# Optimization experiments

Measured on AMD Instinct MI355X. Metric: run time of the kernel, lower is better.

Reference implementation:

```python
import jax, jax.numpy as jnp
import numpy as np


def setup_inputs() -> dict:
    key = jax.random.key(0)
    k_x, k_adj, k_w1, k_b1, k_w2, k_b2 = jax.random.split(key, 6)
    B, S, N, HD = 16, 2048, 64, 32
    x = jax.random.normal(k_x, (B, S, N), dtype=jnp.float32)
    adj = jax.random.uniform(k_adj, (N, N), dtype=jnp.float32)
    # module forces diagonal to 1.0 at init
    adj = adj.at[jnp.arange(N), jnp.arange(N)].set(1.0)
    fc1_w = jax.random.normal(k_w1, (HD, 1), dtype=jnp.float32) * (1.0 / np.sqrt(1.0))
    fc1_b = jax.random.normal(k_b1, (HD,), dtype=jnp.float32) * 0.02
    fc2_w = jax.random.normal(k_w2, (HD, 2 * HD), dtype=jnp.float32) * (1.0 / np.sqrt(2 * HD))
    fc2_b = jax.random.normal(k_b2, (HD,), dtype=jnp.float32) * 0.02
    return {"x": x, "adj": adj, "fc1_w": fc1_w, "fc1_b": fc1_b,
            "fc2_w": fc2_w, "fc2_b": fc2_b}


def reference(x, adj, fc1_w, fc1_b, fc2_w, fc2_b):
    B, S, N = x.shape
    HD = fc1_w.shape[0]
    # row-normalized adjacency
    adj_norm = adj / (adj.sum(axis=1, keepdims=True) + 1e-8)  # [N, N]
    # fc1: Linear(1 -> HD) on x[..., None]; equivalent to outer product + bias
    h = jax.nn.relu(x[..., None] * fc1_w[:, 0] + fc1_b)       # [B, S, N, HD]
    # adjacency-weighted aggregation over variables
    agg = jnp.einsum('ij,bsjf->bsif', adj_norm, h)            # [B, S, N, HD]
    # fc2: Linear(2*HD -> HD) on concat([h, agg])
    h2 = jax.nn.relu(jnp.concatenate([h, agg], axis=-1) @ fc2_w.T + fc2_b)  # [B, S, N, HD]
    # AdaptiveAvgPool1d(1) over seq after permute(0,2,3,1).reshape(B, N*HD, S)
    z = h2.mean(axis=1).reshape(B, N * HD)                    # [B, N*HD]
    return z
```

## Files before the change

kernel.cpp:

```cpp
#include <hip/hip_runtime.h>

#define BN 16
#define SN 2048
#define NV 64
#define HD 32
#define TCH 8
#define SCHUNK 64
#define NSUB (SCHUNK / TCH)
#define CATP 40

typedef short  bf8_t  __attribute__((ext_vector_type(8)));
typedef __bf16 bfv8   __attribute__((ext_vector_type(8)));
typedef __bf16 bfv4   __attribute__((ext_vector_type(4)));
typedef float  f32x16 __attribute__((ext_vector_type(16)));

#define MFMA32(a, b, c) __builtin_amdgcn_mfma_f32_32x32x16_bf16( \
    __builtin_bit_cast(bf8_t, (a)), __builtin_bit_cast(bf8_t, (b)), (c), 0, 0, 0)

__global__ __launch_bounds__(256, 2) void gnn_mfma(
    const float* __restrict__ x,
    const float* __restrict__ adj,
    const float* __restrict__ w1,
    const float* __restrict__ b1,
    const float* __restrict__ w2,
    const float* __restrict__ b2,
    float* __restrict__ out)
{
    __shared__ float  xs[TCH][NV];
    __shared__ __bf16 catg[TCH][NV][CATP];
    __shared__ float  red[NV * HD];
    __shared__ float  rs[NV];

    const int tid  = threadIdx.x;
    const int w    = tid >> 6;
    const int lane = tid & 63;
    const int l31  = lane & 31;
    const int lh   = lane >> 5;
    const int b    = blockIdx.x >> 5;
    const int chk  = blockIdx.x & 31;
    const int sbase = chk * SCHUNK;

    #pragma unroll
    for (int q = 0; q < (NV * HD) / 256; ++q) red[tid + q * 256] = 0.f;

    if (tid < NV) {
        float s = 0.f;
        const float4* r4 = (const float4*)(adj + tid * NV);
        #pragma unroll
        for (int q = 0; q < NV / 4; ++q) { float4 v = r4[q]; s += v.x + v.y + v.z + v.w; }
        rs[tid] = 1.f / (s + 1e-8f);
    }
    __syncthreads();

    bfv8 an[2][4];
    #pragma unroll
    for (int nt = 0; nt < 2; ++nt) {
        const int i = nt * 32 + l31;
        const float rsi = rs[i];
        #pragma unroll
        for (int kk = 0; kk < 4; ++kk) {
            const int j0 = kk * 16 + lh * 8;
            const float4 a0 = *(const float4*)(adj + i * NV + j0);
            const float4 a1 = *(const float4*)(adj + i * NV + j0 + 4);
            bfv8 v;
            v[0] = (__bf16)(a0.x * rsi); v[1] = (__bf16)(a0.y * rsi);
            v[2] = (__bf16)(a0.z * rsi); v[3] = (__bf16)(a0.w * rsi);
            v[4] = (__bf16)(a1.x * rsi); v[5] = (__bf16)(a1.y * rsi);
            v[6] = (__bf16)(a1.z * rsi); v[7] = (__bf16)(a1.w * rsi);
            an[nt][kk] = v;
        }
    }

    bfv8 wf[4];
    #pragma unroll
    for (int kk = 0; kk < 4; ++kk) {
        const int k0 = kk * 16 + lh * 8;
        const float4 a0 = *(const float4*)(w2 + l31 * (2 * HD) + k0);
        const float4 a1 = *(const float4*)(w2 + l31 * (2 * HD) + k0 + 4);
        bfv8 v;
        v[0] = (__bf16)a0.x; v[1] = (__bf16)a0.y; v[2] = (__bf16)a0.z; v[3] = (__bf16)a0.w;
        v[4] = (__bf16)a1.x; v[5] = (__bf16)a1.y; v[6] = (__bf16)a1.z; v[7] = (__bf16)a1.w;
        wf[kk] = v;
    }

    const float w1f = w1[l31];
    const float b1f = b1[l31];
    const float b2f = b2[l31];
    float w1k[2][8], b1k[2][8];
    #pragma unroll
    for (int kk = 0; kk < 2; ++kk) {
        const int k0 = kk * 16 + lh * 8;
        #pragma unroll
        for (int e = 0; e < 8; ++e) { w1k[kk][e] = w1[k0 + e]; b1k[kk][e] = b1[k0 + e]; }
    }

    f32x16 macc0, macc1;
    #pragma unroll
    for (int r = 0; r < 16; ++r) { macc0[r] = 0.f; macc1[r] = 0.f; }

    for (int t = 0; t < NSUB; ++t) {
        __syncthreads();
        if (tid < 128) {
            ((float4*)&xs[0][0])[tid] =
                ((const float4*)(x + ((size_t)b * SN + sbase + t * TCH) * (size_t)NV))[tid];
        }
        __syncthreads();

        #pragma unroll
        for (int sp = 0; sp < 2; ++sp) {
            const int sl = 2 * w + sp;
            bfv8 a1f[4];
            #pragma unroll
            for (int kk = 0; kk < 4; ++kk) {
                const int j0 = kk * 16 + lh * 8;
                const float4 xa = *(const float4*)&xs[sl][j0];
                const float4 xb = *(const float4*)&xs[sl][j0 + 4];
                bfv8 v;
                v[0] = (__bf16)fmaxf(xa.x * w1f + b1f, 0.f);
                v[1] = (__bf16)fmaxf(xa.y * w1f + b1f, 0.f);
                v[2] = (__bf16)fmaxf(xa.z * w1f + b1f, 0.f);
                v[3] = (__bf16)fmaxf(xa.w * w1f + b1f, 0.f);
                v[4] = (__bf16)fmaxf(xb.x * w1f + b1f, 0.f);
                v[5] = (__bf16)fmaxf(xb.y * w1f + b1f, 0.f);
                v[6] = (__bf16)fmaxf(xb.z * w1f + b1f, 0.f);
                v[7] = (__bf16)fmaxf(xb.w * w1f + b1f, 0.f);
                a1f[kk] = v;
            }
            #pragma unroll
            for (int nt = 0; nt < 2; ++nt) {
                f32x16 c;
                #pragma unroll
                for (int r = 0; r < 16; ++r) c[r] = 0.f;
                #pragma unroll
                for (int kk = 0; kk < 4; ++kk) c = MFMA32(a1f[kk], an[nt][kk], c);
                const int i = nt * 32 + l31;
                #pragma unroll
                for (int g = 0; g < 4; ++g) {
                    const int f0 = g * 8 + 4 * lh;
                    bfv4 pv;
                    pv[0] = (__bf16)c[g * 4 + 0]; pv[1] = (__bf16)c[g * 4 + 1];
                    pv[2] = (__bf16)c[g * 4 + 2]; pv[3] = (__bf16)c[g * 4 + 3];
                    *(bfv4*)&catg[sl][i][f0] = pv;
                }
            }
        }

        #pragma unroll
        for (int p = 0; p < 4; ++p) {
            const int mt = 4 * w + p;
            const int sl = mt >> 1;
            const int ih = mt & 1;
            const int i  = ih * 32 + l31;
            const float xv = xs[sl][i];
            f32x16 c;
            #pragma unroll
            for (int r = 0; r < 16; ++r) c[r] = 0.f;
            #pragma unroll
            for (int kk = 0; kk < 2; ++kk) {
                bfv8 v;
                #pragma unroll
                for (int e = 0; e < 8; ++e)
                    v[e] = (__bf16)fmaxf(xv * w1k[kk][e] + b1k[kk][e], 0.f);
                c = MFMA32(v, wf[kk], c);
            }
            #pragma unroll
            for (int kk = 2; kk < 4; ++kk) {
                bfv8 v = *(const bfv8*)&catg[sl][i][(kk - 2) * 16 + lh * 8];
                c = MFMA32(v, wf[kk], c);
            }
            #pragma unroll
            for (int r = 0; r < 16; ++r) {
                const float h2 = fmaxf(c[r] + b2f, 0.f);
                if (ih == 0) macc0[r] += h2; else macc1[r] += h2;
            }
        }
    }

    #pragma unroll
    for (int r = 0; r < 16; ++r) {
        const int row = (r & 3) + 8 * (r >> 2) + 4 * lh;
        atomicAdd(&red[row * HD + l31], macc0[r]);
        atomicAdd(&red[(row + 32) * HD + l31], macc1[r]);
    }
    __syncthreads();
    const float inv = 1.f / (float)SN;
    #pragma unroll
    for (int q = 0; q < (NV * HD) / 256; ++q) {
        const int e = tid + q * 256;
        atomicAdd(out + (size_t)b * (NV * HD) + e, red[e] * inv);
    }
}

extern "C" void kernel_launch(void* const* d_in, const int* in_sizes, int n_in,
                              void* d_out, int out_size, void* d_ws, size_t ws_size,
                              hipStream_t stream) {
    const float* x   = (const float*)d_in[0];
    const float* adj = (const float*)d_in[1];
    const float* w1  = (const float*)d_in[2];
    const float* b1  = (const float*)d_in[3];
    const float* w2  = (const float*)d_in[4];
    const float* b2  = (const float*)d_in[5];
    float* out = (float*)d_out;

    hipMemsetAsync(out, 0, (size_t)out_size * sizeof(float), stream);
    gnn_mfma<<<dim3(BN * 32), dim3(256), 0, stream>>>(x, adj, w1, b1, w2, b2, out);
}
```

Before: 114.8 us.

## Give each wave its own timestep, drop shared x staging and block barriers

Each wave now handles one timestep per iteration and reads x straight from global memory instead of staging it in LDS, so the two __syncthreads per sub-step go away and every wave works on its own catg slice. The grid doubles to 1024 blocks with half the sequence chunk each, and the occupancy hint rises to four blocks per CU. The catg padding shrinks to 36, so reads are split into two 4-element loads. The cost is more blocks doing the per-block adjacency/weight setup and more global atomics in the final reduction.

Result: slower. 184.7 us (+60.8%).

```diff
diff --git a/kernel.cpp b/kernel.cpp
--- a/kernel.cpp
+++ b/kernel.cpp
@@ -4,10 +4,10 @@
 #define SN 2048
 #define NV 64
 #define HD 32
-#define TCH 8
-#define SCHUNK 64
+#define TCH 4
+#define SCHUNK 32
 #define NSUB (SCHUNK / TCH)
-#define CATP 40
+#define CATP 36
 
 typedef short  bf8_t  __attribute__((ext_vector_type(8)));
 typedef __bf16 bfv8   __attribute__((ext_vector_type(8)));
@@ -17,7 +17,7 @@
 #define MFMA32(a, b, c) __builtin_amdgcn_mfma_f32_32x32x16_bf16( \
     __builtin_bit_cast(bf8_t, (a)), __builtin_bit_cast(bf8_t, (b)), (c), 0, 0, 0)
 
-__global__ __launch_bounds__(256, 2) void gnn_mfma(
+__global__ __launch_bounds__(256, 4) void gnn_mfma(
     const float* __restrict__ x,
     const float* __restrict__ adj,
     const float* __restrict__ w1,
@@ -26,7 +26,6 @@
     const float* __restrict__ b2,
     float* __restrict__ out)
 {
-    __shared__ float  xs[TCH][NV];
     __shared__ __bf16 catg[TCH][NV][CATP];
     __shared__ float  red[NV * HD];
     __shared__ float  rs[NV];
@@ -36,8 +35,8 @@
     const int lane = tid & 63;
     const int l31  = lane & 31;
     const int lh   = lane >> 5;
-    const int b    = blockIdx.x >> 5;
-    const int chk  = blockIdx.x & 31;
+    const int b    = blockIdx.x >> 6;
+    const int chk  = blockIdx.x & 63;
     const int sbase = chk * SCHUNK;
 
     #pragma unroll
@@ -99,59 +98,48 @@
     for (int r = 0; r < 16; ++r) { macc0[r] = 0.f; macc1[r] = 0.f; }
 
     for (int t = 0; t < NSUB; ++t) {
-        __syncthreads();
-        if (tid < 128) {
-            ((float4*)&xs[0][0])[tid] =
-                ((const float4*)(x + ((size_t)b * SN + sbase + t * TCH) * (size_t)NV))[tid];
-        }
-        __syncthreads();
-
-        #pragma unroll
-        for (int sp = 0; sp < 2; ++sp) {
-            const int sl = 2 * w + sp;
-            bfv8 a1f[4];
-            #pragma unroll
-            for (int kk = 0; kk < 4; ++kk) {
-                const int j0 = kk * 16 + lh * 8;
-                const float4 xa = *(const float4*)&xs[sl][j0];
-                const float4 xb = *(const float4*)&xs[sl][j0 + 4];
-                bfv8 v;
-                v[0] = (__bf16)fmaxf(xa.x * w1f + b1f, 0.f);
-                v[1] = (__bf16)fmaxf(xa.y * w1f + b1f, 0.f);
-                v[2] = (__bf16)fmaxf(xa.z * w1f + b1f, 0.f);
-                v[3] = (__bf16)fmaxf(xa.w * w1f + b1f, 0.f);
-                v[4] = (__bf16)fmaxf(xb.x * w1f + b1f, 0.f);
-                v[5] = (__bf16)fmaxf(xb.y * w1f + b1f, 0.f);
-                v[6] = (__bf16)fmaxf(xb.z * w1f + b1f, 0.f);
-                v[7] = (__bf16)fmaxf(xb.w * w1f + b1f, 0.f);
-                a1f[kk] = v;
-            }
-            #pragma unroll
-            for (int nt = 0; nt < 2; ++nt) {
-                f32x16 c;
-                #pragma unroll
-                for (int r = 0; r < 16; ++r) c[r] = 0.f;
-                #pragma unroll
-                for (int kk = 0; kk < 4; ++kk) c = MFMA32(a1f[kk], an[nt][kk], c);
-                const int i = nt * 32 + l31;
-                #pragma unroll
-                for (int g = 0; g < 4; ++g) {
-                    const int f0 = g * 8 + 4 * lh;
-                    bfv4 pv;
-                    pv[0] = (__bf16)c[g * 4 + 0]; pv[1] = (__bf16)c[g * 4 + 1];
-                    pv[2] = (__bf16)c[g * 4 + 2]; pv[3] = (__bf16)c[g * 4 + 3];
-                    *(bfv4*)&catg[sl][i][f0] = pv;
-                }
-            }
-        }
-
-        #pragma unroll
-        for (int p = 0; p < 4; ++p) {
-            const int mt = 4 * w + p;
-            const int sl = mt >> 1;
-            const int ih = mt & 1;
+        const float* xp = x + ((size_t)b * SN + sbase + t * TCH + w) * (size_t)NV;
+
+        bfv8 a1f[4];
+        #pragma unroll
+        for (int kk = 0; kk < 4; ++kk) {
+            const int j0 = kk * 16 + lh * 8;
+            const float4 xa = *(const float4*)(xp + j0);
+            const float4 xb = *(const float4*)(xp + j0 + 4);
+            bfv8 v;
+            v[0] = (__bf16)fmaxf(xa.x * w1f + b1f, 0.f);
+            v[1] = (__bf16)fmaxf(xa.y * w1f + b1f, 0.f);
+            v[2] = (__bf16)fmaxf(xa.z * w1f + b1f, 0.f);
+            v[3] = (__bf16)fmaxf(xa.w * w1f + b1f, 0.f);
+            v[4] = (__bf16)fmaxf(xb.x * w1f + b1f, 0.f);
+            v[5] = (__bf16)fmaxf(xb.y * w1f + b1f, 0.f);
+            v[6] = (__bf16)fmaxf(xb.z * w1f + b1f, 0.f);
+            v[7] = (__bf16)fmaxf(xb.w * w1f + b1f, 0.f);
+            a1f[kk] = v;
+        }
+        #pragma unroll
+        for (int nt = 0; nt < 2; ++nt) {
+            f32x16 c;
+            #pragma unroll
+            for (int r = 0; r < 16; ++r) c[r] = 0.f;
+            #pragma unroll
+            for (int kk = 0; kk < 4; ++kk) c = MFMA32(a1f[kk], an[nt][kk], c);
+            const int i = nt * 32 + l31;
+            #pragma unroll
+            for (int g = 0; g < 4; ++g) {
+                const int f0 = g * 8 + 4 * lh;
+                bfv4 pv;
+                pv[0] = (__bf16)c[g * 4 + 0]; pv[1] = (__bf16)c[g * 4 + 1];
+                pv[2] = (__bf16)c[g * 4 + 2]; pv[3] = (__bf16)c[g * 4 + 3];
+                *(bfv4*)&catg[w][i][f0] = pv;
+            }
+        }
+
+        #pragma unroll
+        for (int p = 0; p < 2; ++p) {
+            const int ih = p;
             const int i  = ih * 32 + l31;
-            const float xv = xs[sl][i];
+            const float xv = xp[i];
             f32x16 c;
             #pragma unroll
             for (int r = 0; r < 16; ++r) c[r] = 0.f;
@@ -165,13 +153,18 @@
             }
             #pragma unroll
             for (int kk = 2; kk < 4; ++kk) {
-                bfv8 v = *(const bfv8*)&catg[sl][i][(kk - 2) * 16 + lh * 8];
+                const int f0 = (kk - 2) * 16 + lh * 8;
+                const bfv4 lo = *(const bfv4*)&catg[w][i][f0];
+                const bfv4 hi = *(const bfv4*)&catg[w][i][f0 + 4];
+                bfv8 v;
+                #pragma unroll
+                for (int e = 0; e < 4; ++e) { v[e] = lo[e]; v[e + 4] = hi[e]; }
                 c = MFMA32(v, wf[kk], c);
             }
             #pragma unroll
             for (int r = 0; r < 16; ++r) {
                 const float h2 = fmaxf(c[r] + b2f, 0.f);
-                if (ih == 0) macc0[r] += h2; else macc1[r] += h2;
+                if (p == 0) macc0[r] += h2; else macc1[r] += h2;
             }
         }
     }
@@ -203,5 +196,5 @@
     float* out = (float*)d_out;
 
     hipMemsetAsync(out, 0, (size_t)out_size * sizeof(float), stream);
-    gnn_mfma<<<dim3(BN * 32), dim3(256), 0, stream>>>(x, adj, w1, b1, w2, b2, out);
+    gnn_mfma<<<dim3(BN * 64), dim3(256), 0, stream>>>(x, adj, w1, b1, w2, b2, out);
 }
```
